# Performance work log

Hardware: AMD Instinct MI355X
Metric: run time of the kernel (lower is better)

Reference implementation:

```python
import jax, jax.numpy as jnp
from jax import lax
import numpy as np

B, C, H, W = 4, 256, 64, 64
OC = 256
KH = KW = 3
K = KH * KW  # num_points
STRIDE, PAD, DIL = 1, 1, 1


def setup_inputs() -> dict:
    key = jax.random.key(0)
    k1, k2, k3, k4, k5 = jax.random.split(key, 5)
    x = jax.random.normal(k1, (B, C, H, W), dtype=jnp.float32)
    # offset/mask predictor conv: 3*K channels (dx, dy, mask logits). Small init so
    # offsets stay a few pixels (original inits to zero; we want nontrivial sampling).
    offset_w = jax.random.normal(k2, (3 * K, C, KH, KW), dtype=jnp.float32) * 0.01
    offset_b = jax.random.normal(k3, (3 * K,), dtype=jnp.float32) * 0.01
    fan_in = C * K
    bound = 1.0 / np.sqrt(fan_in)
    weight = jax.random.uniform(k4, (OC, C, KH, KW), dtype=jnp.float32, minval=-bound, maxval=bound)
    bias = jax.random.uniform(k5, (OC,), dtype=jnp.float32, minval=-bound, maxval=bound)
    return {"x": x, "offset_w": offset_w, "offset_b": offset_b, "weight": weight, "bias": bias}


def _bilinear_gather(x, sx, sy):
    """grid_sample(mode=bilinear, padding_mode=zeros, align_corners=True).
    x: [B,C,H,W]; sx, sy: [B,K,P] pixel-space coords. Returns [B,C,K,P].
    (align_corners=True normalize->denormalize is the identity, so we work in pixels.)
    """
    b, c, h, w = x.shape
    xf = x.reshape(b, c, h * w)
    x0 = jnp.floor(sx)
    y0 = jnp.floor(sy)
    wx1 = sx - x0
    wy1 = sy - y0
    wx0 = 1.0 - wx1
    wy0 = 1.0 - wy1

    def corner(xi, yi, wgt):
        valid = (xi >= 0) & (xi <= w - 1) & (yi >= 0) & (yi <= h - 1)
        xc = jnp.clip(xi, 0, w - 1).astype(jnp.int32)
        yc = jnp.clip(yi, 0, h - 1).astype(jnp.int32)
        idx = (yc * w + xc).reshape(b, 1, -1)  # [B,1,K*P]
        v = jnp.take_along_axis(xf, idx, axis=2).reshape(b, c, *xi.shape[1:])
        return v * (wgt * valid.astype(x.dtype))[:, None]

    out = corner(x0, y0, wx0 * wy0)
    out = out + corner(x0 + 1, y0, wx1 * wy0)
    out = out + corner(x0, y0 + 1, wx0 * wy1)
    out = out + corner(x0 + 1, y0 + 1, wx1 * wy1)
    return out


def reference(x, offset_w, offset_b, weight, bias):
    b, c, h, w = x.shape
    om = lax.conv_general_dilated(
        x, offset_w, window_strides=(STRIDE, STRIDE), padding=[(PAD, PAD), (PAD, PAD)],
        rhs_dilation=(DIL, DIL), dimension_numbers=("NCHW", "OIHW", "NCHW"))
    om = om + offset_b[None, :, None, None]
    o1, o2, m = jnp.split(om, 3, axis=1)  # each [B,K,Ho,Wo]
    ho, wo = om.shape[2], om.shape[3]
    p = ho * wo
    offx = o1.reshape(b, K, p)
    offy = o2.reshape(b, K, p)
    mask = jax.nn.sigmoid(m).reshape(b, K, p)

    # kernel grid offsets (-1..1 for k=3) and output pixel positions
    gy, gx = jnp.meshgrid(jnp.arange(-(KH // 2), KH // 2 + 1, dtype=x.dtype),
                          jnp.arange(-(KW // 2), KW // 2 + 1, dtype=x.dtype), indexing="ij")
    gx = gx.reshape(K)
    gy = gy.reshape(K)
    oy, ox = jnp.meshgrid(jnp.arange(ho, dtype=x.dtype), jnp.arange(wo, dtype=x.dtype), indexing="ij")
    ox = ox.reshape(p)
    oy = oy.reshape(p)

    sx = ox[None, None, :] * STRIDE - PAD + gx[None, :, None] * DIL + offx  # [B,K,P]
    sy = oy[None, None, :] * STRIDE - PAD + gy[None, :, None] * DIL + offy

    sampled = _bilinear_gather(x, sx, sy)            # [B,C,K,P]
    sampled = sampled * mask[:, None]                # modulation

    wmat = weight.reshape(OC, c * K)                 # [O, C*K]
    out = jnp.einsum("oi,bip->bop", wmat, sampled.reshape(b, c * K, p))
    out = out.reshape(b, OC, ho, wo) + bias[None, :, None, None]
    return out
```

## Files before the change

### kernel.cpp

```cpp
#include <hip/hip_runtime.h>


#define NB 4
#define NC 256
#define HW 64
#define NP 4096
#define NOC 256
#define NCK 2304
#define NKT 72
#define ROWB 4608

typedef __attribute__((ext_vector_type(8))) short short8;
typedef __attribute__((ext_vector_type(4))) float f32x4;
typedef unsigned short ushort_t;
typedef unsigned int uint32;

__device__ __forceinline__ void gload16(const void* g, void* l) {
    __builtin_amdgcn_global_load_lds(
        (const __attribute__((address_space(1))) unsigned int*)g,
        (__attribute__((address_space(3))) unsigned int*)l, 16, 0, 0);
}

__device__ __forceinline__ uint32 f2bf(float v) {
    uint32 b = __float_as_uint(v);
    return (b + 0x7FFFu + ((b >> 16) & 1u)) >> 16;
}
__device__ __forceinline__ float bf_lo(uint32 u) { return __uint_as_float(u << 16); }
__device__ __forceinline__ float bf_hi(uint32 u) { return __uint_as_float(u & 0xFFFF0000u); }

__global__ __launch_bounds__(256) void wprep_A(const float* __restrict__ w,
                                               ushort_t* __restrict__ wta) {
    int e = blockIdx.x * 256 + threadIdx.x;
    int o  = e / NCK;
    int ck = e - o * NCK;
    int c = ck & 255;
    int k = ck >> 8;
    wta[e] = (ushort_t)f2bf(w[o * NCK + c * 9 + k]);
}

__global__ __launch_bounds__(256) void owb_prep(const float* __restrict__ ow,
                                                ushort_t* __restrict__ owb) {
    int e = blockIdx.x * 256 + threadIdx.x;
    int c = e & 255;
    int r = e >> 8;
    int ch = r & 31;
    int k = r >> 5;
    float v = 0.f;
    if (ch < 27) v = ow[(ch * NC + c) * 9 + k];
    owb[e] = (ushort_t)f2bf(v);
}

__global__ __launch_bounds__(256) void om_init(const float* __restrict__ obias,
                                               float* __restrict__ om) {
    int g = blockIdx.x * 256 + threadIdx.x;
    int r = g >> 12;
    int ch = r % 27;
    om[g] = obias[ch];
}

__global__ __launch_bounds__(256) void xprep2(const float* __restrict__ x,
                                              ushort_t* __restrict__ xt) {
    __shared__ float tr[128 * 65];
    int bid = blockIdx.x;
    int pt = bid & 31;
    int cc = (bid >> 5) & 3;
    int b  = bid >> 7;
    int t = threadIdx.x;
    int c0 = cc * 64;

    const float* xb = x + ((size_t)(b * NC + c0)) * NP + pt * 128;
    #pragma unroll
    for (int pass = 0; pass < 8; ++pass) {
        int c  = pass * 8 + (t >> 5);
        int p4 = (t & 31) * 4;
        float4 v = *(const float4*)(xb + (size_t)c * NP + p4);
        tr[(p4 + 0) * 65 + c] = v.x;
        tr[(p4 + 1) * 65 + c] = v.y;
        tr[(p4 + 2) * 65 + c] = v.z;
        tr[(p4 + 3) * 65 + c] = v.w;
    }
    __syncthreads();
    ushort_t* xto = xt + ((size_t)b * NP + pt * 128) * NC + c0;
    #pragma unroll
    for (int pass = 0; pass < 4; ++pass) {
        int e = pass * 256 + t;
        int p = e >> 3, seg = e & 7;
        const float* rp = &tr[p * 65 + seg * 8];
        uint32 pk[4];
        #pragma unroll
        for (int h = 0; h < 4; ++h)
            pk[h] = f2bf(rp[2 * h]) | (f2bf(rp[2 * h + 1]) << 16);
        *(uint4*)(xto + (size_t)p * NC + seg * 8) = make_uint4(pk[0], pk[1], pk[2], pk[3]);
    }
}

__global__ __launch_bounds__(256) void offs_mfma2(const ushort_t* __restrict__ xt,
                                                  const ushort_t* __restrict__ owb,
                                                  float* __restrict__ om) {
    __shared__ __align__(16) char lds[65376];
    int bid = blockIdx.x;
    int h = bid & 1;
    int y = (bid >> 1) & 63;
    int b = bid >> 7;
    int t = threadIdx.x;
    int lane = t & 63;
    int w = t >> 6;
    int r16 = lane & 15;
    int g   = lane >> 4;

    f32x4 acc[2][4];
    #pragma unroll
    for (int mf = 0; mf < 2; ++mf)
        #pragma unroll
        for (int nf = 0; nf < 4; ++nf) acc[mf][nf] = (f32x4){0.f, 0.f, 0.f, 0.f};

    const ushort_t* xtb = xt + ((size_t)b * NP) * NC;

    for (int ccc = 0; ccc < 2; ++ccc) {
        int c0 = (h * 2 + ccc) * 64;
        __syncthreads();
        for (int e = t; e < 1584; e += 256) {
            int rr = e >> 3, seg = e & 7;
            int dy = (rr >= 132) ? 2 : (rr >= 66 ? 1 : 0);
            int xx = rr - dy * 66;
            int ys = y + dy - 1;
            int xs = xx - 1;
            uint4 v = make_uint4(0, 0, 0, 0);
            if (ys >= 0 && ys < 64 && xs >= 0 && xs < 64)
                v = *(const uint4*)(xtb + ((ys << 6) + xs) * NC + c0 + seg * 8);
            *(uint4*)(lds + rr * 144 + seg * 16) = v;
        }
        for (int e = t; e < 2304; e += 256) {
            int row = e >> 3;
            int seg = e & 7;
            uint4 v = *(const uint4*)(owb + (row << 8) + c0 + seg * 8);
            *(uint4*)(lds + 28512 + (row << 7) + seg * 16) = v;
        }
        __syncthreads();
        for (int s = w; s < 9; s += 4) {
            int dy = (s >= 6) ? 2 : (s >= 3 ? 1 : 0);
            int dx = s - dy * 3;
            const char* Ab = lds + 28512 + s * 4096;
            #pragma unroll
            for (int ks = 0; ks < 2; ++ks) {
                short8 a0 = *(const short8*)(Ab + r16 * 128 + ks * 64 + g * 16);
                short8 a1 = *(const short8*)(Ab + (16 + r16) * 128 + ks * 64 + g * 16);
                #pragma unroll
                for (int nf = 0; nf < 4; ++nf) {
                    short8 bv = *(const short8*)(lds +
                        (dy * 66 + nf * 16 + r16 + dx) * 144 + ks * 64 + g * 16);
                    acc[0][nf] = __builtin_amdgcn_mfma_f32_16x16x32_bf16(
                        a0, bv, acc[0][nf], 0, 0, 0);
                    acc[1][nf] = __builtin_amdgcn_mfma_f32_16x16x32_bf16(
                        a1, bv, acc[1][nf], 0, 0, 0);
                }
            }
        }
    }
    __syncthreads();
    float* red = (float*)lds;
    #pragma unroll
    for (int mf = 0; mf < 2; ++mf)
        #pragma unroll
        for (int nf = 0; nf < 4; ++nf)
            #pragma unroll
            for (int r = 0; r < 4; ++r) {
                int ch = mf * 16 + g * 4 + r;
                int p  = nf * 16 + r16;
                red[((w * 32 + ch) << 6) + p] = acc[mf][nf][r];
            }
    __syncthreads();
    for (int e = t; e < 27 * 64; e += 256) {
        int ch = e >> 6, p = e & 63;
        float sres = red[(ch << 6) + p] + red[((32 + ch) << 6) + p]
                   + red[((64 + ch) << 6) + p] + red[((96 + ch) << 6) + p];
        atomicAdd(&om[((size_t)(b * 27 + ch)) * NP + (y << 6) + p], sres);
    }
}

__global__ __launch_bounds__(256) void gather3(const ushort_t* __restrict__ xt,
                                               const float* __restrict__ om,
                                               ushort_t* __restrict__ sb) {
    __shared__ __align__(16) int4   ci_l[64];
    __shared__ __align__(16) float4 cw_l[64];
    int g = blockIdx.x;
    int b = (g & 7) >> 1;
    int r = ((g >> 3) << 1) | (g & 1);
    int y = r & 63;
    int k = r >> 6;
    int t = threadIdx.x;

    if (t < 64) {
        int p = y * HW + t;
        const float* omb = om + ((size_t)b * 27) * NP;
        float o1 = omb[(size_t)k * NP + p];
        float o2 = omb[(size_t)(9 + k) * NP + p];
        float ml = omb[(size_t)(18 + k) * NP + p];
        float mask = 1.f / (1.f + expf(-ml));
        float sx = (float)t + (float)(k % 3) - 2.0f + o1;
        float sy = (float)y + (float)(k / 3) - 2.0f + o2;
        float x0f = floorf(sx), y0f = floorf(sy);
        float fx = sx - x0f, fy = sy - y0f;
        int idv[4]; float wgt[4];
        #pragma unroll
        for (int cy = 0; cy < 2; ++cy) {
            float yf = y0f + (float)cy;
            float wy = cy ? fy : 1.f - fy;
            #pragma unroll
            for (int cx = 0; cx < 2; ++cx) {
                float xf = x0f + (float)cx;
                float wx = cx ? fx : 1.f - fx;
                bool valid = (xf >= 0.f) && (xf <= 63.f) && (yf >= 0.f) && (yf <= 63.f);
                int xi = min(max((int)xf, 0), 63);
                int yi = min(max((int)yf, 0), 63);
                idv[cy * 2 + cx] = yi * HW + xi;
                wgt[cy * 2 + cx] = valid ? wx * wy * mask : 0.f;
            }
        }
        ci_l[t] = make_int4(idv[0], idv[1], idv[2], idv[3]);
        cw_l[t] = make_float4(wgt[0], wgt[1], wgt[2], wgt[3]);
    }
    __syncthreads();

    int lane = t & 63;
    int w = t >> 6;
    int half = lane >> 5;
    int co = (lane & 31) * 8;
    const ushort_t* xtb = xt + ((size_t)b * NP) * NC + co;
    ushort_t* sbb = sb + ((size_t)b * NP + (size_t)y * HW) * NCK + k * NC + co;

    #pragma unroll 1
    for (int i = 0; i < 8; ++i) {
        int pl = w * 16 + half * 8 + i;
        int4   id = ci_l[pl];
        float4 cw = cw_l[pl];
        uint4 q0 = *(const uint4*)(xtb + (size_t)id.x * NC);
        uint4 q1 = *(const uint4*)(xtb + (size_t)id.y * NC);
        uint4 q2 = *(const uint4*)(xtb + (size_t)id.z * NC);
        uint4 q3 = *(const uint4*)(xtb + (size_t)id.w * NC);
        uint32 a0[4] = {q0.x, q0.y, q0.z, q0.w};
        uint32 a1[4] = {q1.x, q1.y, q1.z, q1.w};
        uint32 a2[4] = {q2.x, q2.y, q2.z, q2.w};
        uint32 a3[4] = {q3.x, q3.y, q3.z, q3.w};
        uint32 pk[4];
        #pragma unroll
        for (int d = 0; d < 4; ++d) {
            float lo = cw.x*bf_lo(a0[d]) + cw.y*bf_lo(a1[d])
                     + cw.z*bf_lo(a2[d]) + cw.w*bf_lo(a3[d]);
            float hi = cw.x*bf_hi(a0[d]) + cw.y*bf_hi(a1[d])
                     + cw.z*bf_hi(a2[d]) + cw.w*bf_hi(a3[d]);
            pk[d] = f2bf(lo) | (f2bf(hi) << 16);
        }
        *(uint4*)(sbb + (size_t)pl * NCK) = make_uint4(pk[0], pk[1], pk[2], pk[3]);
    }
}

__global__ __launch_bounds__(256) void gemm2(const ushort_t* __restrict__ wta,
                                             const ushort_t* __restrict__ sb,
                                             const float* __restrict__ bias,
                                             float* __restrict__ out) {
    __shared__ __align__(16) char lds[2 * 15360];
    int bid = blockIdx.x;
    int pt = bid & 63;
    int ot = (bid >> 6) & 1;
    int b  = bid >> 7;
    int t = threadIdx.x;
    int lane = t & 63;
    int w = t >> 6;
    int wo = w & 1;
    int wp = w >> 1;
    int r16 = lane & 15;
    int g   = lane >> 4;

    const char* Abase = (const char*)wta + (size_t)(ot * 128) * ROWB;
    const char* Bbase = (const char*)sb + (size_t)b * NP * ROWB
                                        + (size_t)(pt * 64) * ROWB;
    const char* srcp[4]; int dstp[4]; bool jv[4];
    #pragma unroll
    for (int jj = 0; jj < 4; ++jj) {
        int j = w + jj * 4;
        jv[jj] = (j < 15);
        if (j < 10) {
            int d = j * 1024 + lane * 16;
            int row = d / 80, col = d - row * 80;
            if (col >= 64) col = 48;
            srcp[jj] = Abase + (size_t)row * ROWB + col;
            dstp[jj] = j * 1024;
        } else if (j < 15) {
            int j2 = j - 10;
            int d = j2 * 1024 + lane * 16;
            int row = d / 80, col = d - row * 80;
            if (col >= 64) col = 48;
            srcp[jj] = Bbase + (size_t)row * ROWB + col;
            dstp[jj] = 10240 + j2 * 1024;
        } else { srcp[jj] = Abase; dstp[jj] = 0; }
    }

    int aoff[4], boff[2];
    #pragma unroll
    for (int f = 0; f < 4; ++f)
        aoff[f] = (wo * 64 + f * 16 + r16) * 80 + g * 16;
    #pragma unroll
    for (int f = 0; f < 2; ++f)
        boff[f] = 10240 + (wp * 32 + f * 16 + r16) * 80 + g * 16;

    f32x4 acc[4][2];
    #pragma unroll
    for (int fo = 0; fo < 4; ++fo)
        #pragma unroll
        for (int fp = 0; fp < 2; ++fp) acc[fo][fp] = (f32x4){0.f, 0.f, 0.f, 0.f};

    #pragma unroll
    for (int jj = 0; jj < 4; ++jj)
        if (jv[jj]) gload16(srcp[jj], lds + dstp[jj]);
    __syncthreads();

    for (int kt = 0; kt < NKT; ++kt) {
        int q = kt & 1;
        if (kt + 1 < NKT) {
            char* dst = lds + (q ^ 1) * 15360;
            size_t ko = (size_t)(kt + 1) * 64;
            #pragma unroll
            for (int jj = 0; jj < 4; ++jj)
                if (jv[jj]) gload16(srcp[jj] + ko, dst + dstp[jj]);
        }
        const char* buf = lds + q * 15360;
        short8 av[4], bv[2];
        #pragma unroll
        for (int f = 0; f < 4; ++f) av[f] = *(const short8*)(buf + aoff[f]);
        #pragma unroll
        for (int f = 0; f < 2; ++f) bv[f] = *(const short8*)(buf + boff[f]);
        #pragma unroll
        for (int fo = 0; fo < 4; ++fo)
            #pragma unroll
            for (int fp = 0; fp < 2; ++fp)
                acc[fo][fp] = __builtin_amdgcn_mfma_f32_16x16x32_bf16(
                    av[fo], bv[fp], acc[fo][fp], 0, 0, 0);
        __syncthreads();
    }

    int obase = ot * 128 + wo * 64;
    int pbase = pt * 64 + wp * 32 + r16;
    float* outb = out + ((size_t)b * NOC) * NP;
    #pragma unroll
    for (int fo = 0; fo < 4; ++fo) {
        #pragma unroll
        for (int rr = 0; rr < 4; ++rr) {
            int o = obase + fo * 16 + g * 4 + rr;
            float bb = bias[o];
            #pragma unroll
            for (int fp = 0; fp < 2; ++fp)
                outb[(size_t)o * NP + pbase + fp * 16] = acc[fo][fp][rr] + bb;
        }
    }
}

extern "C" void kernel_launch(void* const* d_in, const int* in_sizes, int n_in,
                              void* d_out, int out_size, void* d_ws, size_t ws_size,
                              hipStream_t stream) {
    const float* x     = (const float*)d_in[0];
    const float* ow    = (const float*)d_in[1];
    const float* obias = (const float*)d_in[2];
    const float* wgt   = (const float*)d_in[3];
    const float* bias  = (const float*)d_in[4];
    float* out = (float*)d_out;

    char* ws = (char*)d_ws;
    float*    om   = (float*)ws;
    ushort_t* owb  = (ushort_t*)(ws + 1769472);
    ushort_t* wta  = (ushort_t*)(ws + 1916928);
    ushort_t* xt   = (ushort_t*)(ws + 3096576);
    ushort_t* sbuf = (ushort_t*)(ws + 11485184);

    hipLaunchKernelGGL(wprep_A,    dim3(2304), dim3(256), 0, stream, wgt, wta);
    hipLaunchKernelGGL(owb_prep,   dim3(288),  dim3(256), 0, stream, ow, owb);
    hipLaunchKernelGGL(om_init,    dim3(1728), dim3(256), 0, stream, obias, om);
    hipLaunchKernelGGL(xprep2,     dim3(512),  dim3(256), 0, stream, x, xt);
    hipLaunchKernelGGL(offs_mfma2, dim3(512),  dim3(256), 0, stream, xt, owb, om);
    hipLaunchKernelGGL(gather3,    dim3(2304), dim3(256), 0, stream, xt, om, sbuf);
    hipLaunchKernelGGL(gemm2,      dim3(512),  dim3(256), 0, stream, wta, sbuf, bias, out);
}
```

Measured before the change: 168.9 us.

## Fuse bilinear gather into GEMM, producing sampled tiles directly in LDS

Replaces the separate gather kernel and GEMM kernel with one fused kernel. Each 512-thread block handles a full output row of 64 pixels and all 256 output channels, building the bilinear-sampled B tile in LDS for each K-slice while the MFMA runs on the previous slice. The weight tile is streamed with async global-to-LDS loads. This removes the large intermediate sampled buffer and its write and re-read through HBM, plus one launch. In exchange the grid shrinks to 256 blocks at one block per CU, the whole weight matrix is reloaded by every block, and each K step now waits on gather latency.

```diff
diff --git a/kernel.cpp b/kernel.cpp
--- a/kernel.cpp
+++ b/kernel.cpp
@@ -7,8 +7,8 @@
 #define NP 4096
 #define NOC 256
 #define NCK 2304
-#define NKT 72
 #define ROWB 4608
+#define NKT2 36
 
 typedef __attribute__((ext_vector_type(8))) short short8;
 typedef __attribute__((ext_vector_type(4))) float f32x4;
@@ -178,27 +178,39 @@
     }
 }
 
-__global__ __launch_bounds__(256) void gather3(const ushort_t* __restrict__ xt,
-                                               const float* __restrict__ om,
-                                               ushort_t* __restrict__ sb) {
-    __shared__ __align__(16) int4   ci_l[64];
-    __shared__ __align__(16) float4 cw_l[64];
-    int g = blockIdx.x;
-    int b = (g & 7) >> 1;
-    int r = ((g >> 3) << 1) | (g & 1);
-    int y = r & 63;
-    int k = r >> 6;
-    int t = threadIdx.x;
-
-    if (t < 64) {
-        int p = y * HW + t;
+__global__ __launch_bounds__(512, 1) void dcn_main(const ushort_t* __restrict__ wta,
+                                                   const ushort_t* __restrict__ xt,
+                                                   const float* __restrict__ om,
+                                                   const float* __restrict__ bias,
+                                                   float* __restrict__ out) {
+    __shared__ __align__(16) char lds[110592];
+    char*   ldsA = lds;
+    char*   ldsB = lds + 73728;
+    int4*   ci_l = (int4*)(lds + 92160);
+    float4* cw_l = (float4*)(lds + 101376);
+
+    int bid = blockIdx.x;
+    int b  = (bid & 7) >> 1;
+    int pt = ((bid >> 3) << 1) | (bid & 1);
+    int t  = threadIdx.x;
+    int lane = t & 63;
+    int w  = t >> 6;
+    int wo = w & 3;
+    int wp = w >> 2;
+    int r16 = lane & 15;
+    int g   = lane >> 4;
+
+    for (int e = t; e < 576; e += 512) {
+        int k  = e >> 6;
+        int pl = e & 63;
+        int p  = (pt << 6) + pl;
         const float* omb = om + ((size_t)b * 27) * NP;
         float o1 = omb[(size_t)k * NP + p];
         float o2 = omb[(size_t)(9 + k) * NP + p];
         float ml = omb[(size_t)(18 + k) * NP + p];
         float mask = 1.f / (1.f + expf(-ml));
-        float sx = (float)t + (float)(k % 3) - 2.0f + o1;
-        float sy = (float)y + (float)(k / 3) - 2.0f + o2;
+        float sx = (float)pl + (float)(k % 3) - 2.0f + o1;
+        float sy = (float)pt + (float)(k / 3) - 2.0f + o2;
         float x0f = floorf(sx), y0f = floorf(sy);
         float fx = sx - x0f, fy = sy - y0f;
         int idv[4]; float wgt[4];
@@ -217,27 +229,38 @@
                 wgt[cy * 2 + cx] = valid ? wx * wy * mask : 0.f;
             }
         }
-        ci_l[t] = make_int4(idv[0], idv[1], idv[2], idv[3]);
-        cw_l[t] = make_float4(wgt[0], wgt[1], wgt[2], wgt[3]);
-    }
-    __syncthreads();
-
-    int lane = t & 63;
-    int w = t >> 6;
-    int half = lane >> 5;
-    int co = (lane & 31) * 8;
-    const ushort_t* xtb = xt + ((size_t)b * NP) * NC + co;
-    ushort_t* sbb = sb + ((size_t)b * NP + (size_t)y * HW) * NCK + k * NC + co;
-
-    #pragma unroll 1
-    for (int i = 0; i < 8; ++i) {
-        int pl = w * 16 + half * 8 + i;
+        ci_l[e] = make_int4(idv[0], idv[1], idv[2], idv[3]);
+        cw_l[e] = make_float4(wgt[0], wgt[1], wgt[2], wgt[3]);
+    }
+    __syncthreads();
+
+    const ushort_t* xtb = xt + ((size_t)b * NP) * NC;
+    int pl = lane;
+
+    f32x4 acc[4][2];
+    #pragma unroll
+    for (int fo = 0; fo < 4; ++fo)
+        #pragma unroll
+        for (int fp = 0; fp < 2; ++fp) acc[fo][fp] = (f32x4){0.f, 0.f, 0.f, 0.f};
+
+    {
+        #pragma unroll
+        for (int j = 0; j < 5; ++j) {
+            int chunk = j * 512 + t;
+            if (chunk < 2304) {
+                int row  = chunk / 9;
+                int slot = chunk - row * 9; if (slot > 7) slot = 7;
+                gload16((const char*)wta + (size_t)row * ROWB + slot * 16,
+                        ldsA + chunk * 16);
+            }
+        }
         int4   id = ci_l[pl];
-        float4 cw = cw_l[pl];
-        uint4 q0 = *(const uint4*)(xtb + (size_t)id.x * NC);
-        uint4 q1 = *(const uint4*)(xtb + (size_t)id.y * NC);
-        uint4 q2 = *(const uint4*)(xtb + (size_t)id.z * NC);
-        uint4 q3 = *(const uint4*)(xtb + (size_t)id.w * NC);
+        float4 cwv = cw_l[pl];
+        const ushort_t* xb = xtb + w * 8;
+        uint4 q0 = *(const uint4*)(xb + (size_t)id.x * NC);
+        uint4 q1 = *(const uint4*)(xb + (size_t)id.y * NC);
+        uint4 q2 = *(const uint4*)(xb + (size_t)id.z * NC);
+        uint4 q3 = *(const uint4*)(xb + (size_t)id.w * NC);
         uint32 a0[4] = {q0.x, q0.y, q0.z, q0.w};
         uint32 a1[4] = {q1.x, q1.y, q1.z, q1.w};
         uint32 a2[4] = {q2.x, q2.y, q2.z, q2.w};
@@ -245,112 +268,101 @@
         uint32 pk[4];
         #pragma unroll
         for (int d = 0; d < 4; ++d) {
-            float lo = cw.x*bf_lo(a0[d]) + cw.y*bf_lo(a1[d])
-                     + cw.z*bf_lo(a2[d]) + cw.w*bf_lo(a3[d]);
-            float hi = cw.x*bf_hi(a0[d]) + cw.y*bf_hi(a1[d])
-                     + cw.z*bf_hi(a2[d]) + cw.w*bf_hi(a3[d]);
+            float lo = cwv.x*bf_lo(a0[d]) + cwv.y*bf_lo(a1[d])
+                     + cwv.z*bf_lo(a2[d]) + cwv.w*bf_lo(a3[d]);
+            float hi = cwv.x*bf_hi(a0[d]) + cwv.y*bf_hi(a1[d])
+                     + cwv.z*bf_hi(a2[d]) + cwv.w*bf_hi(a3[d]);
             pk[d] = f2bf(lo) | (f2bf(hi) << 16);
         }
-        *(uint4*)(sbb + (size_t)pl * NCK) = make_uint4(pk[0], pk[1], pk[2], pk[3]);
-    }
-}
-
-__global__ __launch_bounds__(256) void gemm2(const ushort_t* __restrict__ wta,
-                                             const ushort_t* __restrict__ sb,
-                                             const float* __restrict__ bias,
-                                             float* __restrict__ out) {
-    __shared__ __align__(16) char lds[2 * 15360];
-    int bid = blockIdx.x;
-    int pt = bid & 63;
-    int ot = (bid >> 6) & 1;
-    int b  = bid >> 7;
-    int t = threadIdx.x;
-    int lane = t & 63;
-    int w = t >> 6;
-    int wo = w & 1;
-    int wp = w >> 1;
-    int r16 = lane & 15;
-    int g   = lane >> 4;
-
-    const char* Abase = (const char*)wta + (size_t)(ot * 128) * ROWB;
-    const char* Bbase = (const char*)sb + (size_t)b * NP * ROWB
-                                        + (size_t)(pt * 64) * ROWB;
-    const char* srcp[4]; int dstp[4]; bool jv[4];
-    #pragma unroll
-    for (int jj = 0; jj < 4; ++jj) {
-        int j = w + jj * 4;
-        jv[jj] = (j < 15);
-        if (j < 10) {
-            int d = j * 1024 + lane * 16;
-            int row = d / 80, col = d - row * 80;
-            if (col >= 64) col = 48;
-            srcp[jj] = Abase + (size_t)row * ROWB + col;
-            dstp[jj] = j * 1024;
-        } else if (j < 15) {
-            int j2 = j - 10;
-            int d = j2 * 1024 + lane * 16;
-            int row = d / 80, col = d - row * 80;
-            if (col >= 64) col = 48;
-            srcp[jj] = Bbase + (size_t)row * ROWB + col;
-            dstp[jj] = 10240 + j2 * 1024;
-        } else { srcp[jj] = Abase; dstp[jj] = 0; }
-    }
-
-    int aoff[4], boff[2];
-    #pragma unroll
-    for (int f = 0; f < 4; ++f)
-        aoff[f] = (wo * 64 + f * 16 + r16) * 80 + g * 16;
-    #pragma unroll
-    for (int f = 0; f < 2; ++f)
-        boff[f] = 10240 + (wp * 32 + f * 16 + r16) * 80 + g * 16;
-
-    f32x4 acc[4][2];
-    #pragma unroll
-    for (int fo = 0; fo < 4; ++fo)
-        #pragma unroll
-        for (int fp = 0; fp < 2; ++fp) acc[fo][fp] = (f32x4){0.f, 0.f, 0.f, 0.f};
-
-    #pragma unroll
-    for (int jj = 0; jj < 4; ++jj)
-        if (jv[jj]) gload16(srcp[jj], lds + dstp[jj]);
-    __syncthreads();
-
-    for (int kt = 0; kt < NKT; ++kt) {
-        int q = kt & 1;
-        if (kt + 1 < NKT) {
-            char* dst = lds + (q ^ 1) * 15360;
-            size_t ko = (size_t)(kt + 1) * 64;
-            #pragma unroll
-            for (int jj = 0; jj < 4; ++jj)
-                if (jv[jj]) gload16(srcp[jj] + ko, dst + dstp[jj]);
-        }
-        const char* buf = lds + q * 15360;
-        short8 av[4], bv[2];
-        #pragma unroll
-        for (int f = 0; f < 4; ++f) av[f] = *(const short8*)(buf + aoff[f]);
-        #pragma unroll
-        for (int f = 0; f < 2; ++f) bv[f] = *(const short8*)(buf + boff[f]);
-        #pragma unroll
-        for (int fo = 0; fo < 4; ++fo)
+        *(uint4*)(ldsB + pl * 144 + w * 16) = make_uint4(pk[0], pk[1], pk[2], pk[3]);
+    }
+    __syncthreads();
+
+    for (int kt = 0; kt < NKT2; ++kt) {
+        int cur = kt & 1;
+        uint4 q0, q1, q2, q3; float4 cwv;
+        bool has_next = (kt + 1) < NKT2;
+        if (has_next) {
+            char* dstA = ldsA + (cur ^ 1) * 36864;
+            #pragma unroll
+            for (int j = 0; j < 5; ++j) {
+                int chunk = j * 512 + t;
+                if (chunk < 2304) {
+                    int row  = chunk / 9;
+                    int slot = chunk - row * 9; if (slot > 7) slot = 7;
+                    gload16((const char*)wta + (size_t)row * ROWB
+                                + (size_t)(kt + 1) * 128 + slot * 16,
+                            dstA + chunk * 16);
+                }
+            }
+            int kk = (kt + 1) >> 2;
+            int c0 = ((kt + 1) & 3) * 64;
+            int4 id = ci_l[kk * 64 + pl];
+            cwv = cw_l[kk * 64 + pl];
+            const ushort_t* xb = xtb + c0 + w * 8;
+            q0 = *(const uint4*)(xb + (size_t)id.x * NC);
+            q1 = *(const uint4*)(xb + (size_t)id.y * NC);
+            q2 = *(const uint4*)(xb + (size_t)id.z * NC);
+            q3 = *(const uint4*)(xb + (size_t)id.w * NC);
+        }
+
+        {
+            const char* A  = ldsA + cur * 36864;
+            const char* Bt = ldsB + cur * 9216;
+            short8 av[2][4], bv[2][2];
+            #pragma unroll
+            for (int ks = 0; ks < 2; ++ks) {
+                #pragma unroll
+                for (int fo = 0; fo < 4; ++fo)
+                    av[ks][fo] = *(const short8*)(A + (wo * 64 + fo * 16 + r16) * 144
+                                                    + ks * 64 + g * 16);
+                #pragma unroll
+                for (int fp = 0; fp < 2; ++fp)
+                    bv[ks][fp] = *(const short8*)(Bt + (wp * 32 + fp * 16 + r16) * 144
+                                                     + ks * 64 + g * 16);
+            }
+            __builtin_amdgcn_s_setprio(1);
+            #pragma unroll
+            for (int ks = 0; ks < 2; ++ks)
+                #pragma unroll
+                for (int fo = 0; fo < 4; ++fo)
+                    #pragma unroll
+                    for (int fp = 0; fp < 2; ++fp)
+                        acc[fo][fp] = __builtin_amdgcn_mfma_f32_16x16x32_bf16(
+                            av[ks][fo], bv[ks][fp], acc[fo][fp], 0, 0, 0);
+            __builtin_amdgcn_s_setprio(0);
+        }
+
+        if (has_next) {
+            uint32 a0[4] = {q0.x, q0.y, q0.z, q0.w};
+            uint32 a1[4] = {q1.x, q1.y, q1.z, q1.w};
+            uint32 a2[4] = {q2.x, q2.y, q2.z, q2.w};
+            uint32 a3[4] = {q3.x, q3.y, q3.z, q3.w};
+            uint32 pk[4];
+            #pragma unroll
+            for (int d = 0; d < 4; ++d) {
+                float lo = cwv.x*bf_lo(a0[d]) + cwv.y*bf_lo(a1[d])
+                         + cwv.z*bf_lo(a2[d]) + cwv.w*bf_lo(a3[d]);
+                float hi = cwv.x*bf_hi(a0[d]) + cwv.y*bf_hi(a1[d])
+                         + cwv.z*bf_hi(a2[d]) + cwv.w*bf_hi(a3[d]);
+                pk[d] = f2bf(lo) | (f2bf(hi) << 16);
+            }
+            *(uint4*)(ldsB + (cur ^ 1) * 9216 + pl * 144 + w * 16) =
+                make_uint4(pk[0], pk[1], pk[2], pk[3]);
+        }
+        __syncthreads();
+    }
+
+    float* outb = out + ((size_t)b * NOC) * NP + (pt << 6);
+    #pragma unroll
+    for (int fo = 0; fo < 4; ++fo) {
+        #pragma unroll
+        for (int rr = 0; rr < 4; ++rr) {
+            int o = wo * 64 + fo * 16 + g * 4 + rr;
+            float bb = bias[o];
             #pragma unroll
             for (int fp = 0; fp < 2; ++fp)
-                acc[fo][fp] = __builtin_amdgcn_mfma_f32_16x16x32_bf16(
-                    av[fo], bv[fp], acc[fo][fp], 0, 0, 0);
-        __syncthreads();
-    }
-
-    int obase = ot * 128 + wo * 64;
-    int pbase = pt * 64 + wp * 32 + r16;
-    float* outb = out + ((size_t)b * NOC) * NP;
-    #pragma unroll
-    for (int fo = 0; fo < 4; ++fo) {
-        #pragma unroll
-        for (int rr = 0; rr < 4; ++rr) {
-            int o = obase + fo * 16 + g * 4 + rr;
-            float bb = bias[o];
-            #pragma unroll
-            for (int fp = 0; fp < 2; ++fp)
-                outb[(size_t)o * NP + pbase + fp * 16] = acc[fo][fp][rr] + bb;
+                outb[(size_t)o * NP + wp * 32 + fp * 16 + r16] = acc[fo][fp][rr] + bb;
         }
     }
 }
@@ -370,13 +382,11 @@
     ushort_t* owb  = (ushort_t*)(ws + 1769472);
     ushort_t* wta  = (ushort_t*)(ws + 1916928);
     ushort_t* xt   = (ushort_t*)(ws + 3096576);
-    ushort_t* sbuf = (ushort_t*)(ws + 11485184);
 
     hipLaunchKernelGGL(wprep_A,    dim3(2304), dim3(256), 0, stream, wgt, wta);
     hipLaunchKernelGGL(owb_prep,   dim3(288),  dim3(256), 0, stream, ow, owb);
     hipLaunchKernelGGL(om_init,    dim3(1728), dim3(256), 0, stream, obias, om);
     hipLaunchKernelGGL(xprep2,     dim3(512),  dim3(256), 0, stream, x, xt);
     hipLaunchKernelGGL(offs_mfma2, dim3(512),  dim3(256), 0, stream, xt, owb, om);
-    hipLaunchKernelGGL(gather3,    dim3(2304), dim3(256), 0, stream, xt, om, sbuf);
-    hipLaunchKernelGGL(gemm2,      dim3(512),  dim3(256), 0, stream, wta, sbuf, bias, out);
-}
+    hipLaunchKernelGGL(dcn_main,   dim3(256),  dim3(512), 0, stream, wta, xt, om, bias, out);
+}
```

Result: no change. 169.7 us (+0.5%).
